# Optimization experiments

Measured on AMD Instinct MI355X. Metric: run time of the kernel, lower is better.

The kernel has to match this reference:

```python
import jax, jax.numpy as jnp
import numpy as np


def setup_inputs() -> dict:
    key = jax.random.key(0)
    k1, k2, k3, k4 = jax.random.split(key, 4)
    B, C, H, W = 16, 256, 128, 128
    fft_features = jax.random.normal(k1, (B, C, H, W), dtype=jnp.float32)
    multi_features = jax.random.normal(k2, (B, C, H, W), dtype=jnp.float32)
    # 1x1 convs without bias == dense layers on pooled channel vector
    # Conv2d(2C, C//4): weight [C//4, 2C]; Conv2d(C//4, 2C): weight [2C, C//4]
    w1 = jax.random.normal(k3, (C // 4, 2 * C), dtype=jnp.float32) * (1.0 / np.sqrt(2 * C))
    w2 = jax.random.normal(k4, (2 * C, C // 4), dtype=jnp.float32) * (1.0 / np.sqrt(C // 4))
    return {"fft_features": fft_features, "multi_features": multi_features, "w1": w1, "w2": w2}


def reference(fft_features, multi_features, w1, w2):
    C = fft_features.shape[1]
    # global average pool over H, W of the (implicit) concat -> [B, 2C]
    pooled = jnp.concatenate(
        [fft_features.mean(axis=(2, 3)), multi_features.mean(axis=(2, 3))], axis=1
    )
    # two 1x1 convs on 1x1 spatial == tiny GEMMs
    h = jax.nn.relu(jnp.einsum("bc,rc->br", pooled, w1))  # [B, C/4]
    attn = jax.nn.sigmoid(jnp.einsum("br,cr->bc", h, w2))  # [B, 2C]
    fft_w = attn[:, :C][:, :, None, None]
    multi_w = attn[:, C:][:, :, None, None]
    return fft_w * fft_features + multi_w * multi_features
```

## Files before the change

kernel.cpp:

```cpp
#include <hip/hip_runtime.h>

#define HW 16384
#define NC 256
#define NB 16

typedef float floatx4 __attribute__((ext_vector_type(4)));

__device__ __forceinline__ float sum4(floatx4 v) { return (v.x + v.y) + (v.z + v.w); }
__device__ __forceinline__ floatx4 ntload(const floatx4* p) {
    return __builtin_nontemporal_load(p);
}


__global__ __launch_bounds__(256, 4) void pool_kernel(const float* __restrict__ fft,
                                                      const float* __restrict__ multi,
                                                      float* __restrict__ pooled) {
    int bc = blockIdx.x;
    int tid = threadIdx.x;
    int lane = tid & 63, wid = tid >> 6;
    const floatx4* fbase = (const floatx4*)fft + ((size_t)bc << 12) + tid;
    const floatx4* mbase = (const floatx4*)multi + ((size_t)bc << 12) + tid;

    float fs0 = 0.f, fs1 = 0.f, fs2 = 0.f, fs3 = 0.f;
    float fs4 = 0.f, fs5 = 0.f, fs6 = 0.f, fs7 = 0.f;
    float ms0 = 0.f, ms1 = 0.f, ms2 = 0.f, ms3 = 0.f;
    float ms4 = 0.f, ms5 = 0.f, ms6 = 0.f, ms7 = 0.f;

#pragma unroll
    for (int chunk = 0; chunk < 2; ++chunk) {
        const floatx4* pf = fbase + chunk * 2048;
        const floatx4* pm = mbase + chunk * 2048;
        floatx4 f0 = ntload(pf + 0),    f1 = ntload(pf + 256);
        floatx4 f2 = ntload(pf + 512),  f3 = ntload(pf + 768);
        floatx4 f4 = ntload(pf + 1024), f5 = ntload(pf + 1280);
        floatx4 f6 = ntload(pf + 1536), f7 = ntload(pf + 1792);
        floatx4 m0 = ntload(pm + 0),    m1 = ntload(pm + 256);
        floatx4 m2 = ntload(pm + 512),  m3 = ntload(pm + 768);
        floatx4 m4 = ntload(pm + 1024), m5 = ntload(pm + 1280);
        floatx4 m6 = ntload(pm + 1536), m7 = ntload(pm + 1792);
        fs0 += sum4(f0); fs1 += sum4(f1); fs2 += sum4(f2); fs3 += sum4(f3);
        fs4 += sum4(f4); fs5 += sum4(f5); fs6 += sum4(f6); fs7 += sum4(f7);
        ms0 += sum4(m0); ms1 += sum4(m1); ms2 += sum4(m2); ms3 += sum4(m3);
        ms4 += sum4(m4); ms5 += sum4(m5); ms6 += sum4(m6); ms7 += sum4(m7);
    }
    float fsum = ((fs0 + fs1) + (fs2 + fs3)) + ((fs4 + fs5) + (fs6 + fs7));
    float msum = ((ms0 + ms1) + (ms2 + ms3)) + ((ms4 + ms5) + (ms6 + ms7));

#pragma unroll
    for (int off = 32; off > 0; off >>= 1) {
        fsum += __shfl_xor(fsum, off, 64);
        msum += __shfl_xor(msum, off, 64);
    }

    __shared__ float ws[4][2];
    if (lane == 0) { ws[wid][0] = fsum; ws[wid][1] = msum; }
    __syncthreads();
    if (tid < 2) {
        float s = (ws[0][tid] + ws[1][tid]) + (ws[2][tid] + ws[3][tid]);
        int b = bc >> 8, c = bc & 255;
        pooled[b * 512 + tid * 256 + c] = s * (1.0f / HW);
    }
}

__global__ __launch_bounds__(256) void mlp1_kernel(const float* __restrict__ pooled,
                                                   const float* __restrict__ w1,
                                                   float* __restrict__ h) {
    int wid = (blockIdx.x << 2) | (threadIdx.x >> 6);
    int lane = threadIdx.x & 63;
    int b = wid >> 6, r = wid & 63;
    const float4* w = (const float4*)(w1 + (size_t)r * 512) + (lane << 1);
    const float4* p = (const float4*)(pooled + b * 512) + (lane << 1);
    float4 wa = w[0], wb = w[1];
    float4 pa = p[0], pb = p[1];
    float s = wa.x * pa.x + wa.y * pa.y + wa.z * pa.z + wa.w * pa.w
            + wb.x * pb.x + wb.y * pb.y + wb.z * pb.z + wb.w * pb.w;
#pragma unroll
    for (int off = 32; off > 0; off >>= 1) s += __shfl_xor(s, off, 64);
    if (lane == 0) h[wid] = fmaxf(s, 0.f);
}

__global__ __launch_bounds__(256) void mlp2_kernel(const float* __restrict__ h,
                                                   const float* __restrict__ w2,
                                                   float* __restrict__ attn) {
    int wid = (blockIdx.x << 2) | (threadIdx.x >> 6);
    int lane = threadIdx.x & 63;
    int b = wid >> 9, c = wid & 511;
    float s = h[(b << 6) | lane] * w2[((size_t)c << 6) | lane];
#pragma unroll
    for (int off = 32; off > 0; off >>= 1) s += __shfl_xor(s, off, 64);
    if (lane == 0) attn[(b << 9) | c] = 1.0f / (1.0f + __expf(-s));
}

__global__ __launch_bounds__(256) void apply_kernel(const float* __restrict__ fft,
                                                    const float* __restrict__ multi,
                                                    const float* __restrict__ attn,
                                                    float* __restrict__ out) {
    int g = blockIdx.x;
    int tid = threadIdx.x;

#pragma unroll
    for (int pl = 0; pl < 2; ++pl) {
        int plane = (g << 1) | pl;
        int b = plane >> 8, c = plane & 255;
        float fw = attn[b * 512 + c];
        float mw = attn[b * 512 + 256 + c];
        const floatx4* pf = (const floatx4*)fft + ((size_t)plane << 12) + tid;
        const floatx4* pm = (const floatx4*)multi + ((size_t)plane << 12) + tid;
        floatx4* po = (floatx4*)out + ((size_t)plane << 12) + tid;

#pragma unroll
        for (int it = 0; it < 4; ++it) {
            const floatx4* qf = pf + it * 1024;
            const floatx4* qm = pm + it * 1024;
            floatx4* qo = po + it * 1024;
            floatx4 f0 = ntload(qf + 0),   f1 = ntload(qf + 256);
            floatx4 f2 = ntload(qf + 512), f3 = ntload(qf + 768);
            floatx4 m0 = ntload(qm + 0),   m1 = ntload(qm + 256);
            floatx4 m2 = ntload(qm + 512), m3 = ntload(qm + 768);
            floatx4 o0, o1, o2, o3;
            o0.x = fmaf(fw, f0.x, mw * m0.x); o0.y = fmaf(fw, f0.y, mw * m0.y);
            o0.z = fmaf(fw, f0.z, mw * m0.z); o0.w = fmaf(fw, f0.w, mw * m0.w);
            o1.x = fmaf(fw, f1.x, mw * m1.x); o1.y = fmaf(fw, f1.y, mw * m1.y);
            o1.z = fmaf(fw, f1.z, mw * m1.z); o1.w = fmaf(fw, f1.w, mw * m1.w);
            o2.x = fmaf(fw, f2.x, mw * m2.x); o2.y = fmaf(fw, f2.y, mw * m2.y);
            o2.z = fmaf(fw, f2.z, mw * m2.z); o2.w = fmaf(fw, f2.w, mw * m2.w);
            o3.x = fmaf(fw, f3.x, mw * m3.x); o3.y = fmaf(fw, f3.y, mw * m3.y);
            o3.z = fmaf(fw, f3.z, mw * m3.z); o3.w = fmaf(fw, f3.w, mw * m3.w);
            qo[0]   = o0;
            qo[256] = o1;
            qo[512] = o2;
            qo[768] = o3;
        }
    }
}

extern "C" void kernel_launch(void* const* d_in, const int* in_sizes, int n_in,
                              void* d_out, int out_size, void* d_ws, size_t ws_size,
                              hipStream_t stream) {
    const float* fft   = (const float*)d_in[0];
    const float* multi = (const float*)d_in[1];
    const float* w1    = (const float*)d_in[2];
    const float* w2    = (const float*)d_in[3];
    float* out = (float*)d_out;

    float* pooled = (float*)d_ws;
    float* h      = pooled + NB * 512;
    float* attn   = h + NB * 64;

    pool_kernel<<<4096, 256, 0, stream>>>(fft, multi, pooled);
    mlp1_kernel<<<256, 256, 0, stream>>>(pooled, w1, h);
    mlp2_kernel<<<2048, 256, 0, stream>>>(h, w2, attn);
    apply_kernel<<<2048, 256, 0, stream>>>(fft, multi, attn, out);
}
```

Baseline: 213.5 us.

## Fuse squeeze-excite MLP kernels and give apply kernel one plane per block

Merges the two tiny dense-layer kernels into one per-batch kernel that keeps the hidden vector in shared memory, removing a launch and a global round trip. The apply kernel now processes one channel plane per block with eight vector loads in flight per tensor, doubling the grid size. The fused MLP runs on only 16 blocks, so its serial latency could partly offset the saved launch.

```diff
diff --git a/kernel.cpp b/kernel.cpp
--- a/kernel.cpp
+++ b/kernel.cpp
@@ -62,75 +62,97 @@
     }
 }
 
-__global__ __launch_bounds__(256) void mlp1_kernel(const float* __restrict__ pooled,
-                                                   const float* __restrict__ w1,
-                                                   float* __restrict__ h) {
-    int wid = (blockIdx.x << 2) | (threadIdx.x >> 6);
-    int lane = threadIdx.x & 63;
-    int b = wid >> 6, r = wid & 63;
-    const float4* w = (const float4*)(w1 + (size_t)r * 512) + (lane << 1);
-    const float4* p = (const float4*)(pooled + b * 512) + (lane << 1);
-    float4 wa = w[0], wb = w[1];
-    float4 pa = p[0], pb = p[1];
-    float s = wa.x * pa.x + wa.y * pa.y + wa.z * pa.z + wa.w * pa.w
-            + wb.x * pb.x + wb.y * pb.y + wb.z * pb.z + wb.w * pb.w;
+__global__ __launch_bounds__(256) void mlp_fused_kernel(const float* __restrict__ pooled,
+                                                        const float* __restrict__ w1,
+                                                        const float* __restrict__ w2,
+                                                        float* __restrict__ attn) {
+    __shared__ float h[64];
+    int b = blockIdx.x;
+    int tid = threadIdx.x;
+    int lane = tid & 63, wid = tid >> 6;
+
+    const float4* pb = (const float4*)(pooled + b * 512) + (lane << 1);
+    float4 pa = pb[0], pbv = pb[1];
 #pragma unroll
-    for (int off = 32; off > 0; off >>= 1) s += __shfl_xor(s, off, 64);
-    if (lane == 0) h[wid] = fmaxf(s, 0.f);
-}
+    for (int i = 0; i < 16; ++i) {
+        int r = (wid << 4) | i;
+        const float4* w = (const float4*)(w1 + (size_t)r * 512) + (lane << 1);
+        float4 wa = w[0], wb = w[1];
+        float s = wa.x * pa.x + wa.y * pa.y + wa.z * pa.z + wa.w * pa.w
+                + wb.x * pbv.x + wb.y * pbv.y + wb.z * pbv.z + wb.w * pbv.w;
+#pragma unroll
+        for (int off = 32; off > 0; off >>= 1) s += __shfl_xor(s, off, 64);
+        if (lane == 0) h[r] = fmaxf(s, 0.f);
+    }
+    __syncthreads();
 
-__global__ __launch_bounds__(256) void mlp2_kernel(const float* __restrict__ h,
-                                                   const float* __restrict__ w2,
-                                                   float* __restrict__ attn) {
-    int wid = (blockIdx.x << 2) | (threadIdx.x >> 6);
-    int lane = threadIdx.x & 63;
-    int b = wid >> 9, c = wid & 511;
-    float s = h[(b << 6) | lane] * w2[((size_t)c << 6) | lane];
 #pragma unroll
-    for (int off = 32; off > 0; off >>= 1) s += __shfl_xor(s, off, 64);
-    if (lane == 0) attn[(b << 9) | c] = 1.0f / (1.0f + __expf(-s));
+    for (int half = 0; half < 2; ++half) {
+        int c = (half << 8) | tid;
+        const float4* w = (const float4*)(w2 + ((size_t)c << 6));
+        const float4* hh = (const float4*)h;
+        float s = 0.f;
+#pragma unroll
+        for (int k = 0; k < 16; ++k) {
+            float4 wv = w[k];
+            float4 hv = hh[k];
+            s += wv.x * hv.x + wv.y * hv.y + wv.z * hv.z + wv.w * hv.w;
+        }
+        attn[(b << 9) | c] = 1.0f / (1.0f + __expf(-s));
+    }
 }
 
 __global__ __launch_bounds__(256) void apply_kernel(const float* __restrict__ fft,
                                                     const float* __restrict__ multi,
                                                     const float* __restrict__ attn,
                                                     float* __restrict__ out) {
-    int g = blockIdx.x;
+    int plane = blockIdx.x;
     int tid = threadIdx.x;
+    int b = plane >> 8, c = plane & 255;
+    float fw = attn[b * 512 + c];
+    float mw = attn[b * 512 + 256 + c];
+    const floatx4* pf = (const floatx4*)fft + ((size_t)plane << 12) + tid;
+    const floatx4* pm = (const floatx4*)multi + ((size_t)plane << 12) + tid;
+    floatx4* po = (floatx4*)out + ((size_t)plane << 12) + tid;
 
 #pragma unroll
-    for (int pl = 0; pl < 2; ++pl) {
-        int plane = (g << 1) | pl;
-        int b = plane >> 8, c = plane & 255;
-        float fw = attn[b * 512 + c];
-        float mw = attn[b * 512 + 256 + c];
-        const floatx4* pf = (const floatx4*)fft + ((size_t)plane << 12) + tid;
-        const floatx4* pm = (const floatx4*)multi + ((size_t)plane << 12) + tid;
-        floatx4* po = (floatx4*)out + ((size_t)plane << 12) + tid;
-
-#pragma unroll
-        for (int it = 0; it < 4; ++it) {
-            const floatx4* qf = pf + it * 1024;
-            const floatx4* qm = pm + it * 1024;
-            floatx4* qo = po + it * 1024;
-            floatx4 f0 = ntload(qf + 0),   f1 = ntload(qf + 256);
-            floatx4 f2 = ntload(qf + 512), f3 = ntload(qf + 768);
-            floatx4 m0 = ntload(qm + 0),   m1 = ntload(qm + 256);
-            floatx4 m2 = ntload(qm + 512), m3 = ntload(qm + 768);
-            floatx4 o0, o1, o2, o3;
-            o0.x = fmaf(fw, f0.x, mw * m0.x); o0.y = fmaf(fw, f0.y, mw * m0.y);
-            o0.z = fmaf(fw, f0.z, mw * m0.z); o0.w = fmaf(fw, f0.w, mw * m0.w);
-            o1.x = fmaf(fw, f1.x, mw * m1.x); o1.y = fmaf(fw, f1.y, mw * m1.y);
-            o1.z = fmaf(fw, f1.z, mw * m1.z); o1.w = fmaf(fw, f1.w, mw * m1.w);
-            o2.x = fmaf(fw, f2.x, mw * m2.x); o2.y = fmaf(fw, f2.y, mw * m2.y);
-            o2.z = fmaf(fw, f2.z, mw * m2.z); o2.w = fmaf(fw, f2.w, mw * m2.w);
-            o3.x = fmaf(fw, f3.x, mw * m3.x); o3.y = fmaf(fw, f3.y, mw * m3.y);
-            o3.z = fmaf(fw, f3.z, mw * m3.z); o3.w = fmaf(fw, f3.w, mw * m3.w);
-            qo[0]   = o0;
-            qo[256] = o1;
-            qo[512] = o2;
-            qo[768] = o3;
-        }
+    for (int half = 0; half < 2; ++half) {
+        const floatx4* qf = pf + half * 2048;
+        const floatx4* qm = pm + half * 2048;
+        floatx4* qo = po + half * 2048;
+        floatx4 f0 = ntload(qf + 0),    f1 = ntload(qf + 256);
+        floatx4 f2 = ntload(qf + 512),  f3 = ntload(qf + 768);
+        floatx4 f4 = ntload(qf + 1024), f5 = ntload(qf + 1280);
+        floatx4 f6 = ntload(qf + 1536), f7 = ntload(qf + 1792);
+        floatx4 m0 = ntload(qm + 0),    m1 = ntload(qm + 256);
+        floatx4 m2 = ntload(qm + 512),  m3 = ntload(qm + 768);
+        floatx4 m4 = ntload(qm + 1024), m5 = ntload(qm + 1280);
+        floatx4 m6 = ntload(qm + 1536), m7 = ntload(qm + 1792);
+        floatx4 o0, o1, o2, o3, o4v, o5, o6, o7;
+        o0.x = fmaf(fw, f0.x, mw * m0.x); o0.y = fmaf(fw, f0.y, mw * m0.y);
+        o0.z = fmaf(fw, f0.z, mw * m0.z); o0.w = fmaf(fw, f0.w, mw * m0.w);
+        o1.x = fmaf(fw, f1.x, mw * m1.x); o1.y = fmaf(fw, f1.y, mw * m1.y);
+        o1.z = fmaf(fw, f1.z, mw * m1.z); o1.w = fmaf(fw, f1.w, mw * m1.w);
+        o2.x = fmaf(fw, f2.x, mw * m2.x); o2.y = fmaf(fw, f2.y, mw * m2.y);
+        o2.z = fmaf(fw, f2.z, mw * m2.z); o2.w = fmaf(fw, f2.w, mw * m2.w);
+        o3.x = fmaf(fw, f3.x, mw * m3.x); o3.y = fmaf(fw, f3.y, mw * m3.y);
+        o3.z = fmaf(fw, f3.z, mw * m3.z); o3.w = fmaf(fw, f3.w, mw * m3.w);
+        o4v.x = fmaf(fw, f4.x, mw * m4.x); o4v.y = fmaf(fw, f4.y, mw * m4.y);
+        o4v.z = fmaf(fw, f4.z, mw * m4.z); o4v.w = fmaf(fw, f4.w, mw * m4.w);
+        o5.x = fmaf(fw, f5.x, mw * m5.x); o5.y = fmaf(fw, f5.y, mw * m5.y);
+        o5.z = fmaf(fw, f5.z, mw * m5.z); o5.w = fmaf(fw, f5.w, mw * m5.w);
+        o6.x = fmaf(fw, f6.x, mw * m6.x); o6.y = fmaf(fw, f6.y, mw * m6.y);
+        o6.z = fmaf(fw, f6.z, mw * m6.z); o6.w = fmaf(fw, f6.w, mw * m6.w);
+        o7.x = fmaf(fw, f7.x, mw * m7.x); o7.y = fmaf(fw, f7.y, mw * m7.y);
+        o7.z = fmaf(fw, f7.z, mw * m7.z); o7.w = fmaf(fw, f7.w, mw * m7.w);
+        qo[0]    = o0;
+        qo[256]  = o1;
+        qo[512]  = o2;
+        qo[768]  = o3;
+        qo[1024] = o4v;
+        qo[1280] = o5;
+        qo[1536] = o6;
+        qo[1792] = o7;
     }
 }
 
@@ -144,11 +166,9 @@
     float* out = (float*)d_out;
 
     float* pooled = (float*)d_ws;
-    float* h      = pooled + NB * 512;
-    float* attn   = h + NB * 64;
+    float* attn   = pooled + NB * 512;
 
     pool_kernel<<<4096, 256, 0, stream>>>(fft, multi, pooled);
-    mlp1_kernel<<<256, 256, 0, stream>>>(pooled, w1, h);
-    mlp2_kernel<<<2048, 256, 0, stream>>>(h, w2, attn);
-    apply_kernel<<<2048, 256, 0, stream>>>(fft, multi, attn, out);
+    mlp_fused_kernel<<<NB, 256, 0, stream>>>(pooled, w1, w2, attn);
+    apply_kernel<<<4096, 256, 0, stream>>>(fft, multi, attn, out);
 }
```

Result: no change. 217.3 us (+1.8%).
